# Performance work log

Hardware: AMD Instinct MI355X
Metric: run time of the kernel (lower is better)

Reference implementation:

```python
import jax, jax.numpy as jnp
import numpy as np

L = 64      # lattice side
H = 32      # hiddenSize
D = 2       # inputDim (spin states)
B = 1024    # batch of configurations
LOG_PROB_FACTOR = 0.5


def setup_inputs() -> dict:
    key = jax.random.key(0)
    ks = jax.random.split(key, 6)
    s = 0.3  # uniform init half-width (mimics variance_scaling uniform)
    return {
        "x": jax.random.randint(ks[0], (B, L, L), 0, D, dtype=jnp.int32),
        "Win": jax.random.uniform(ks[1], (2 * D, H), minval=-s, maxval=s, dtype=jnp.float32),
        "WcH": jax.random.uniform(ks[2], (H, H), minval=-s, maxval=s, dtype=jnp.float32),
        "WcV": jax.random.uniform(ks[3], (H, H), minval=-s, maxval=s, dtype=jnp.float32),
        "bV": jnp.zeros((H,), dtype=jnp.float32),
        "Wout": jax.random.uniform(ks[4], (H, D), minval=-s, maxval=s, dtype=jnp.float32),
        "bout": (0.1 * jax.random.normal(ks[5], (D,))).astype(jnp.float32),
    }


def _rev(line, b, axis):
    # reverse_line: identity if direction b == 1 else flip along `axis`
    return jnp.where(b == 1, line, jnp.flip(line, axis=axis))


def reference(x, Win, WcH, WcV, bV, Wout, bout):
    Bn, Ln, _ = x.shape
    d = Wout.shape[1]
    h = WcH.shape[0]
    xoh = jax.nn.one_hot(x, d, dtype=Win.dtype)            # [B, L, L, d]
    direction = jnp.asarray(np.where(np.arange(Ln) % 2 == 0, 1, -1).astype(np.int32))

    def col_step(hcarry, cols):
        # hcarry: horizontal carry [B, h]; cols: (carryV [B,h], stateH [B,d], stateV [B,d])
        cV, sH, sV = cols
        newR = jnp.concatenate([sH, sV], axis=-1)          # [B, 2d]
        newC = jax.nn.elu(hcarry @ WcH + (cV @ WcV + bV) + newR @ Win)  # [B, h]
        out = newC @ Wout + bout                            # [B, d]
        return newC, (newC, jax.nn.log_softmax(out, axis=-1))

    def row_step(carry, inputs):
        carryV_grid, prevRow = carry                        # [B, L, h], [B, L, d]
        x_row, b = inputs                                   # [B, L, d], scalar direction
        cV_rev = _rev(carryV_grid, b, 1)
        x_rev = _rev(x_row, b, 1)
        prev_rev = _rev(prevRow, b, 1)
        # shifted previous-column state along scan direction
        stateH = jnp.concatenate(
            [jnp.zeros((Bn, 1, d), dtype=x_rev.dtype), x_rev], axis=1)[:, :-1]
        xs = (jnp.swapaxes(cV_rev, 0, 1),                   # [L, B, h]
              jnp.swapaxes(stateH, 0, 1),                   # [L, B, d]
              jnp.swapaxes(prev_rev, 0, 1))                 # [L, B, d]
        _, (carries, logsm) = jax.lax.scan(
            col_step, jnp.zeros((Bn, h), dtype=Win.dtype), xs)
        carries = jnp.swapaxes(carries, 0, 1)               # [B, L, h]
        logsm = jnp.swapaxes(logsm, 0, 1)                   # [B, L, d]
        logP = jnp.sum(_rev(logsm, b, 1) * x_row, axis=-1)  # [B, L]
        logP = jnp.nan_to_num(logP, nan=-35.0)
        return (_rev(carries, b, 1), x_row), logP

    init = (jnp.zeros((Bn, Ln, h), dtype=Win.dtype),
            jnp.zeros((Bn, Ln, d), dtype=Win.dtype))
    _, probs = jax.lax.scan(row_step, init, (jnp.moveaxis(xoh, 1, 0), direction))
    # probs: [L_rows, B, L_cols] -> per-sample log-prob
    return LOG_PROB_FACTOR * jnp.sum(probs, axis=(0, 2))   # [B]
```

## Files before the change

### kernel.cpp

```cpp
#include <hip/hip_runtime.h>
#include <cstdint>

namespace {

typedef _Float16 half_t;
typedef half_t half8  __attribute__((ext_vector_type(8)));
typedef __fp16 fp16x2 __attribute__((ext_vector_type(2)));
typedef float  f32x4  __attribute__((ext_vector_type(4)));

constexpr int LSIDE = 64;
constexpr int HID   = 32;
constexpr int NB    = 16;

__device__ __forceinline__ half8 as_h8(uint4 u) { return __builtin_bit_cast(half8, u); }
__device__ __forceinline__ uint4 as_u4(half8 h) { return __builtin_bit_cast(uint4, h); }
__device__ __forceinline__ unsigned pk2(float a, float b) {
    fp16x2 t = __builtin_amdgcn_cvt_pkrtz(a, b);
    return __builtin_bit_cast(unsigned, t);
}
__device__ __forceinline__ float elu1(float v) {
    float e = __expf(v) - 1.f;
    return v > 0.f ? v : e;
}
__device__ __forceinline__ half8 elupack(const f32x4& a1, const f32x4& a2) {
    uint4 nb;
    nb.x = pk2(elu1(a1[0]), elu1(a1[1]));
    nb.y = pk2(elu1(a1[2]), elu1(a1[3]));
    nb.z = pk2(elu1(a2[0]), elu1(a2[1]));
    nb.w = pk2(elu1(a2[2]), elu1(a2[3]));
    return as_h8(nb);
}

#define MFMA(a,b,c) __builtin_amdgcn_mfma_f32_16x16x32_f16((a),(b),(c),0,0,0)


__global__ __launch_bounds__(192) void rnn2d_pipe3(
    const int*   __restrict__ x,
    const float* __restrict__ Win,
    const float* __restrict__ WcH,
    const float* __restrict__ WcV,
    const float* __restrict__ bV,
    const float* __restrict__ Wout,
    const float* __restrict__ bout,
    float*       __restrict__ out)
{
    const int tid = threadIdx.x;
    const int wv  = tid >> 6;
    const int l   = tid & 63;
    const int r_  = l & 15, g_ = l >> 4, n = l & 15;
    const int bbase = blockIdx.x * NB;

    __shared__ uint4 cvs[64 * 64];
    __shared__ f32x4 ring1[4 * 8 * 64];
    __shared__ f32x4 ring2[4 * 8 * 64];
    __shared__ uint4 h7buf[8 * 64];

    for (int i = tid; i < 64 * 64; i += 192) cvs[i] = uint4{0u,0u,0u,0u};

    const int j1 = 8 * (r_ >> 2) + (r_ & 3), j2 = j1 + 4;
    half8 A1h, A2h, A1v, A2v, A3a, A3b, Awd;
#pragma unroll
    for (int e = 0; e < 8; ++e) {
        const int k = 8 * g_ + e;
        A1h[e] = (half_t)WcH[k * HID + j1];
        A2h[e] = (half_t)WcH[k * HID + j2];
        A1v[e] = (half_t)WcV[k * HID + j1];
        A2v[e] = (half_t)WcV[k * HID + j2];
        float a3a = 0.f, a3b = 0.f;
        if (k < 4)       { a3a = Win[k * HID + j1]; a3b = Win[k * HID + j2]; }
        else if (k == 4) { a3a = bV[j1];            a3b = bV[j2]; }
        A3a[e] = (half_t)a3a;
        A3b[e] = (half_t)a3b;
        Awd[e] = (half_t)((r_ == 0) ? (Wout[k * 2 + 1] - Wout[k * 2 + 0]) : 0.f);
    }
    const float db = bout[1] - bout[0];
    f32x4 dinit; dinit[0]=db; dinit[1]=db; dinit[2]=db; dinit[3]=db;
    f32x4 zc;    zc[0]=0.f;  zc[1]=0.f;  zc[2]=0.f;  zc[3]=0.f;
    const unsigned gm16 = (g_ == 0) ? 0x3C00u : 0u;

    const int* xw = x + (long)bbase * 4096;

    __syncthreads();

    unsigned long long rmc = 0ull, rm1 = 0ull;
    int xr[NB];
    float logp = 0.f;
    f32x4 Ua[4], Ub[4];
    half8 hc = as_h8(uint4{0u,0u,0u,0u});
    uint4 h7[8];
#pragma unroll
    for (int i = 0; i < 8; ++i) h7[i] = uint4{0u,0u,0u,0u};

    if (wv >= 1) {
#pragma unroll
        for (int nn = 0; nn < NB; ++nn) xr[nn] = xw[nn * 4096 + l];
        {
            unsigned long long rm = 0ull;
#pragma unroll
            for (int nn = 0; nn < NB; ++nn) {
                unsigned long long bal = __ballot(xr[nn] == 1);
                rm = (n == nn) ? bal : rm;
            }
            rmc = rm;
        }
#pragma unroll
        for (int nn = 0; nn < NB; ++nn) xr[nn] = xw[nn * 4096 + 64 + l];
    }

    if (wv == 1) {
#pragma unroll
        for (int i = 0; i < 8; ++i) {
            unsigned aP = 0u;
            if (i > 0) {
                unsigned bl = (unsigned)((rmc >> (i - 1)) & 1ull);
                aP = gm16 << (bl << 4);
            }
            uint4 b3u{aP, 0u, gm16, 0u};
            ring1[(0*8 + i)*64 + l] = MFMA(A3a, as_h8(b3u), zc);
            ring2[(0*8 + i)*64 + l] = MFMA(A3b, as_h8(b3u), zc);
        }
#pragma unroll
        for (int i = 0; i < 8; ++i) {
            const int c = 8 + i;
            unsigned bl = (unsigned)((rmc >> (c - 1)) & 1ull);
            unsigned aP = gm16 << (bl << 4);
            uint4 b3u{aP, 0u, gm16, 0u};
            ring1[(1*8 + i)*64 + l] = MFMA(A3a, as_h8(b3u), zc);
            ring2[(1*8 + i)*64 + l] = MFMA(A3b, as_h8(b3u), zc);
        }
    }
    __syncthreads();

    if (wv == 0) {
        Ua[0] = ring1[0*64+l]; Ub[0] = ring2[0*64+l];
        Ua[1] = ring1[1*64+l]; Ub[1] = ring2[1*64+l];
        Ua[2] = ring1[2*64+l]; Ub[2] = ring2[2*64+l];
    }

    int c0 = 0, dir0 = 1;

#define PF(i)  { const int pf_=(i)+3; const int cs_=(gph+(pf_>>3))&3; const int ci_=pf_&7; \
                 Ua[((i)+3)&3] = ring1[(cs_*8+ci_)*64+l];                                  \
                 Ub[((i)+3)&3] = ring2[(cs_*8+ci_)*64+l]; }

#define NORMAL(i) { PF(i)                                                                  \
      f32x4 a1 = MFMA(A1h, hc, Ua[(i)&3]); f32x4 a2 = MFMA(A2h, hc, Ub[(i)&3]);           \
      hc = elupack(a1, a2); cvs[c0*64+l] = as_u4(hc); c0 += dir0; }

#define NORM7(i) { PF(i)                                                                   \
      f32x4 a1 = MFMA(A1h, hc, Ua[(i)&3]); f32x4 a2 = MFMA(A2h, hc, Ub[(i)&3]);           \
      hc = elupack(a1, a2); { uint4 u_ = as_u4(hc); cvs[c0*64+l] = u_; h7[(i)] = u_;      \
      h7buf[(i)*64+l] = u_; } c0 += dir0; }

#define SPECIAL(i) { PF(i)                                                                 \
      f32x4 p1 = MFMA(A1v, as_h8(h7[7-(i)]), Ua[(i)&3]);                                   \
      f32x4 p2 = MFMA(A2v, as_h8(h7[7-(i)]), Ub[(i)&3]);                                   \
      f32x4 a1 = MFMA(A1h, hc, p1); f32x4 a2 = MFMA(A2h, hc, p2);                          \
      hc = elupack(a1, a2); cvs[c0*64+l] = as_u4(hc); c0 += dir0; }

    for (int gph = 0; gph < 512; ++gph) {
        if (wv == 0) {
            const int k = gph & 7, rr = gph >> 3;
            if (k == 0) {
                dir0 = (rr & 1) ? -1 : 1;
                c0   = (rr & 1) ? 63 : 0;
                hc   = as_h8(uint4{0u,0u,0u,0u});
                SPECIAL(0) SPECIAL(1) SPECIAL(2) SPECIAL(3)
                SPECIAL(4) SPECIAL(5) SPECIAL(6) SPECIAL(7)
            } else if (k < 7) {
                NORMAL(0) NORMAL(1) NORMAL(2) NORMAL(3)
                NORMAL(4) NORMAL(5) NORMAL(6) NORMAL(7)
            } else {
                NORM7(0) NORM7(1) NORM7(2) NORM7(3)
                NORM7(4) NORM7(5) NORM7(6) NORM7(7)
            }
        } else if (wv == 1) {
            const int t = gph + 2;
            if (t < 512) {
                const int rp = t >> 3, kp = t & 7;
                const int dirp = (rp & 1) ? -1 : 1;
                const int slot = t & 3;
                if (kp == 0) {
                    rm1 = rmc;
                    {
                        unsigned long long rm = 0ull;
#pragma unroll
                        for (int nn = 0; nn < NB; ++nn) {
                            unsigned long long bal = __ballot(xr[nn] == 1);
                            rm = (n == nn) ? bal : rm;
                        }
                        rmc = rm;
                    }
                    const int nr = (rp < 63) ? rp + 1 : 63;
#pragma unroll
                    for (int nn = 0; nn < NB; ++nn) xr[nn] = xw[nn * 4096 + nr * 64 + l];
#pragma unroll
                    for (int i = 0; i < 8; ++i) {
                        const int c = (rp & 1) ? 63 - i : i;
                        unsigned aP = 0u;
                        if (i > 0) {
                            unsigned bl = (unsigned)((rmc >> (c - dirp)) & 1ull);
                            aP = gm16 << (bl << 4);
                        }
                        unsigned bu = (unsigned)((rm1 >> c) & 1ull);
                        unsigned bP = gm16 << (bu << 4);
                        uint4 b3u{aP, bP, gm16, 0u};
                        ring1[(slot*8 + i)*64 + l] = MFMA(A3a, as_h8(b3u), zc);
                        ring2[(slot*8 + i)*64 + l] = MFMA(A3b, as_h8(b3u), zc);
                    }
                } else {
#pragma unroll
                    for (int i = 0; i < 8; ++i) {
                        const int sg = 8 * kp + i;
                        const int c = (rp & 1) ? 63 - sg : sg;
                        half8 cvh = as_h8(cvs[c*64 + l]);
                        unsigned bl = (unsigned)((rmc >> (c - dirp)) & 1ull);
                        unsigned aP = gm16 << (bl << 4);
                        unsigned bP = 0u;
                        if (rp >= 1) {
                            unsigned bu = (unsigned)((rm1 >> c) & 1ull);
                            bP = gm16 << (bu << 4);
                        }
                        uint4 b3u{aP, bP, gm16, 0u};
                        f32x4 q1 = MFMA(A3a, as_h8(b3u), zc);
                        f32x4 q2 = MFMA(A3b, as_h8(b3u), zc);
                        ring1[(slot*8 + i)*64 + l] = MFMA(A1v, cvh, q1);
                        ring2[(slot*8 + i)*64 + l] = MFMA(A2v, cvh, q2);
                    }
                }
            }
        } else {
            const int t = gph + 2;
            if (t < 512) {
                const int rp = t >> 3, kp = t & 7;
                if (kp == 0) {
                    rm1 = rmc;
                    {
                        unsigned long long rm = 0ull;
#pragma unroll
                        for (int nn = 0; nn < NB; ++nn) {
                            unsigned long long bal = __ballot(xr[nn] == 1);
                            rm = (n == nn) ? bal : rm;
                        }
                        rmc = rm;
                    }
                    const int nr = (rp < 63) ? rp + 1 : 63;
#pragma unroll
                    for (int nn = 0; nn < NB; ++nn) xr[nn] = xw[nn * 4096 + nr * 64 + l];
                } else if (rp >= 1) {
                    f32x4 odv[8];
#pragma unroll
                    for (int i = 0; i < 8; ++i) {
                        const int sg = 8 * kp + i;
                        const int c = (rp & 1) ? 63 - sg : sg;
                        odv[i] = MFMA(Awd, as_h8(cvs[c*64 + l]), dinit);
                    }
#pragma unroll
                    for (int i = 0; i < 8; ++i) {
                        const int sg = 8 * kp + i;
                        const int c = (rp & 1) ? 63 - sg : sg;
                        unsigned s32 = (unsigned)((rm1 >> c) & 1ull) << 31;
                        float du = __int_as_float(__float_as_int(odv[i][0]) ^ s32);
                        logp -= __logf(1.f + __expf(du));
                    }
                    if (kp == 2) {
                        f32x4 odt[8];
#pragma unroll
                        for (int i = 0; i < 8; ++i)
                            odt[i] = MFMA(Awd, as_h8(h7buf[i*64 + l]), dinit);
#pragma unroll
                        for (int i = 0; i < 8; ++i) {
                            const int c = ((rp - 1) & 1) ? 7 - i : 56 + i;
                            unsigned s32 = (unsigned)((rm1 >> c) & 1ull) << 31;
                            float du = __int_as_float(__float_as_int(odt[i][0]) ^ s32);
                            logp -= __logf(1.f + __expf(du));
                        }
                    }
                }
            }
        }
        __syncthreads();
    }

    if (wv == 2) {
#pragma unroll 8
        for (int c = 0; c < 64; ++c) {
            f32x4 od = MFMA(Awd, as_h8(cvs[c*64 + l]), dinit);
            unsigned s32 = (unsigned)((rmc >> c) & 1ull) << 31;
            float du = __int_as_float(__float_as_int(od[0]) ^ s32);
            logp -= __logf(1.f + __expf(du));
        }
        if (l < NB) out[bbase + n] = 0.5f * logp;
    }

#undef PF
#undef NORMAL
#undef NORM7
#undef SPECIAL
}

}

extern "C" void kernel_launch(void* const* d_in, const int* in_sizes, int n_in,
                              void* d_out, int out_size, void* d_ws, size_t ws_size,
                              hipStream_t stream) {
    (void)n_in; (void)out_size; (void)d_ws; (void)ws_size;
    const int*   x    = (const int*)  d_in[0];
    const float* Win  = (const float*)d_in[1];
    const float* WcH  = (const float*)d_in[2];
    const float* WcV  = (const float*)d_in[3];
    const float* bV   = (const float*)d_in[4];
    const float* Wout = (const float*)d_in[5];
    const float* bout = (const float*)d_in[6];
    float*       out  = (float*)d_out;

    const int B = in_sizes[0] / (LSIDE * LSIDE);
    rnn2d_pipe3<<<B / NB, 192, 0, stream>>>(x, Win, WcH, WcV, bV, Wout, bout, out);
}
```

Before: 789.7 us.

## Store ELU state shifted by one and fold log2e scaling into weights

The hidden state is stored as s = (elu(v)+1)/ln2-scaled form so that the activation becomes max(v,0)*ln2 + exp2(min(v,0)), computed with a raw exp2 instruction and no select or subtract. The +1 offset and the log2e factor are folded into the weights, the biases (row sums subtracted) and the output bias, and the zero initial carries become ones. The aim is a shorter serial dependency chain in the recurrent critical path. The cost is a more intricate reparameterisation with fp16 rounding of shifted values and scaled weights, plus extra setup reads of the weights. The prefill of the first ring slots now also includes a vertical-carry MFMA over the ones-initialised cvs buffer.

After: 744.8 us. -5.7%, faster.

```diff
diff --git a/kernel.cpp b/kernel.cpp
--- a/kernel.cpp
+++ b/kernel.cpp
@@ -11,6 +11,8 @@
 constexpr int LSIDE = 64;
 constexpr int HID   = 32;
 constexpr int NB    = 16;
+constexpr float LOG2E = 1.4426950408889634f;
+constexpr float LN2   = 0.6931471805599453f;
 
 __device__ __forceinline__ half8 as_h8(uint4 u) { return __builtin_bit_cast(half8, u); }
 __device__ __forceinline__ uint4 as_u4(half8 h) { return __builtin_bit_cast(uint4, h); }
@@ -18,23 +20,27 @@
     fp16x2 t = __builtin_amdgcn_cvt_pkrtz(a, b);
     return __builtin_bit_cast(unsigned, t);
 }
-__device__ __forceinline__ float elu1(float v) {
-    float e = __expf(v) - 1.f;
-    return v > 0.f ? v : e;
-}
-__device__ __forceinline__ half8 elupack(const f32x4& a1, const f32x4& a2) {
+
+__device__ __forceinline__ half8 elupack2(const f32x4& a1, const f32x4& a2) {
+    float m[8], w[8], e[8], s[8];
+#pragma unroll
+    for (int i = 0; i < 4; ++i) { m[i]   = fmaxf(a1[i], 0.f); w[i]   = fminf(a1[i], 0.f); }
+#pragma unroll
+    for (int i = 0; i < 4; ++i) { m[4+i] = fmaxf(a2[i], 0.f); w[4+i] = fminf(a2[i], 0.f); }
+#pragma unroll
+    for (int i = 0; i < 8; ++i) e[i] = __builtin_amdgcn_exp2f(w[i]);
+#pragma unroll
+    for (int i = 0; i < 8; ++i) s[i] = fmaf(m[i], LN2, e[i]);
     uint4 nb;
-    nb.x = pk2(elu1(a1[0]), elu1(a1[1]));
-    nb.y = pk2(elu1(a1[2]), elu1(a1[3]));
-    nb.z = pk2(elu1(a2[0]), elu1(a2[1]));
-    nb.w = pk2(elu1(a2[2]), elu1(a2[3]));
+    nb.x = pk2(s[0], s[1]); nb.y = pk2(s[2], s[3]);
+    nb.z = pk2(s[4], s[5]); nb.w = pk2(s[6], s[7]);
     return as_h8(nb);
 }
 
 #define MFMA(a,b,c) __builtin_amdgcn_mfma_f32_16x16x32_f16((a),(b),(c),0,0,0)
 
 
-__global__ __launch_bounds__(192) void rnn2d_pipe3(
+__global__ __launch_bounds__(192) void rnn2d_pipe4(
     const int*   __restrict__ x,
     const float* __restrict__ Win,
     const float* __restrict__ WcH,
@@ -55,25 +61,36 @@
     __shared__ f32x4 ring2[4 * 8 * 64];
     __shared__ uint4 h7buf[8 * 64];
 
-    for (int i = tid; i < 64 * 64; i += 192) cvs[i] = uint4{0u,0u,0u,0u};
+    const uint4 ONES4{0x3C003C00u, 0x3C003C00u, 0x3C003C00u, 0x3C003C00u};
+    for (int i = tid; i < 64 * 64; i += 192) cvs[i] = ONES4;
 
     const int j1 = 8 * (r_ >> 2) + (r_ & 3), j2 = j1 + 4;
+    float rsH1 = 0.f, rsH2 = 0.f, rsV1 = 0.f, rsV2 = 0.f;
+#pragma unroll
+    for (int k = 0; k < HID; ++k) {
+        rsH1 += WcH[k * HID + j1]; rsH2 += WcH[k * HID + j2];
+        rsV1 += WcV[k * HID + j1]; rsV2 += WcV[k * HID + j2];
+    }
     half8 A1h, A2h, A1v, A2v, A3a, A3b, Awd;
 #pragma unroll
     for (int e = 0; e < 8; ++e) {
         const int k = 8 * g_ + e;
-        A1h[e] = (half_t)WcH[k * HID + j1];
-        A2h[e] = (half_t)WcH[k * HID + j2];
-        A1v[e] = (half_t)WcV[k * HID + j1];
-        A2v[e] = (half_t)WcV[k * HID + j2];
+        A1h[e] = (half_t)(LOG2E * WcH[k * HID + j1]);
+        A2h[e] = (half_t)(LOG2E * WcH[k * HID + j2]);
+        A1v[e] = (half_t)(LOG2E * WcV[k * HID + j1]);
+        A2v[e] = (half_t)(LOG2E * WcV[k * HID + j2]);
         float a3a = 0.f, a3b = 0.f;
         if (k < 4)       { a3a = Win[k * HID + j1]; a3b = Win[k * HID + j2]; }
-        else if (k == 4) { a3a = bV[j1];            a3b = bV[j2]; }
-        A3a[e] = (half_t)a3a;
-        A3b[e] = (half_t)a3b;
+        else if (k == 4) { a3a = bV[j1] - rsH1 - rsV1;
+                           a3b = bV[j2] - rsH2 - rsV2; }
+        A3a[e] = (half_t)(LOG2E * a3a);
+        A3b[e] = (half_t)(LOG2E * a3b);
         Awd[e] = (half_t)((r_ == 0) ? (Wout[k * 2 + 1] - Wout[k * 2 + 0]) : 0.f);
     }
-    const float db = bout[1] - bout[0];
+    float sAwd = 0.f;
+#pragma unroll
+    for (int k = 0; k < HID; ++k) sAwd += Wout[k * 2 + 1] - Wout[k * 2 + 0];
+    const float db = bout[1] - bout[0] - sAwd;
     f32x4 dinit; dinit[0]=db; dinit[1]=db; dinit[2]=db; dinit[3]=db;
     f32x4 zc;    zc[0]=0.f;  zc[1]=0.f;  zc[2]=0.f;  zc[3]=0.f;
     const unsigned gm16 = (g_ == 0) ? 0x3C00u : 0u;
@@ -86,10 +103,10 @@
     int xr[NB];
     float logp = 0.f;
     f32x4 Ua[4], Ub[4];
-    half8 hc = as_h8(uint4{0u,0u,0u,0u});
+    half8 hc = as_h8(ONES4);
     uint4 h7[8];
 #pragma unroll
-    for (int i = 0; i < 8; ++i) h7[i] = uint4{0u,0u,0u,0u};
+    for (int i = 0; i < 8; ++i) h7[i] = ONES4;
 
     if (wv >= 1) {
 #pragma unroll
@@ -125,8 +142,11 @@
             unsigned bl = (unsigned)((rmc >> (c - 1)) & 1ull);
             unsigned aP = gm16 << (bl << 4);
             uint4 b3u{aP, 0u, gm16, 0u};
-            ring1[(1*8 + i)*64 + l] = MFMA(A3a, as_h8(b3u), zc);
-            ring2[(1*8 + i)*64 + l] = MFMA(A3b, as_h8(b3u), zc);
+            f32x4 q1 = MFMA(A3a, as_h8(b3u), zc);
+            f32x4 q2 = MFMA(A3b, as_h8(b3u), zc);
+            half8 cvh = as_h8(cvs[c*64 + l]);
+            ring1[(1*8 + i)*64 + l] = MFMA(A1v, cvh, q1);
+            ring2[(1*8 + i)*64 + l] = MFMA(A2v, cvh, q2);
         }
     }
     __syncthreads();
@@ -145,18 +165,18 @@
 
 #define NORMAL(i) { PF(i)                                                                  \
       f32x4 a1 = MFMA(A1h, hc, Ua[(i)&3]); f32x4 a2 = MFMA(A2h, hc, Ub[(i)&3]);           \
-      hc = elupack(a1, a2); cvs[c0*64+l] = as_u4(hc); c0 += dir0; }
+      hc = elupack2(a1, a2); cvs[c0*64+l] = as_u4(hc); c0 += dir0; }
 
 #define NORM7(i) { PF(i)                                                                   \
       f32x4 a1 = MFMA(A1h, hc, Ua[(i)&3]); f32x4 a2 = MFMA(A2h, hc, Ub[(i)&3]);           \
-      hc = elupack(a1, a2); { uint4 u_ = as_u4(hc); cvs[c0*64+l] = u_; h7[(i)] = u_;      \
+      hc = elupack2(a1, a2); { uint4 u_ = as_u4(hc); cvs[c0*64+l] = u_; h7[(i)] = u_;     \
       h7buf[(i)*64+l] = u_; } c0 += dir0; }
 
 #define SPECIAL(i) { PF(i)                                                                 \
       f32x4 p1 = MFMA(A1v, as_h8(h7[7-(i)]), Ua[(i)&3]);                                   \
       f32x4 p2 = MFMA(A2v, as_h8(h7[7-(i)]), Ub[(i)&3]);                                   \
       f32x4 a1 = MFMA(A1h, hc, p1); f32x4 a2 = MFMA(A2h, hc, p2);                          \
-      hc = elupack(a1, a2); cvs[c0*64+l] = as_u4(hc); c0 += dir0; }
+      hc = elupack2(a1, a2); cvs[c0*64+l] = as_u4(hc); c0 += dir0; }
 
     for (int gph = 0; gph < 512; ++gph) {
         if (wv == 0) {
@@ -164,7 +184,7 @@
             if (k == 0) {
                 dir0 = (rr & 1) ? -1 : 1;
                 c0   = (rr & 1) ? 63 : 0;
-                hc   = as_h8(uint4{0u,0u,0u,0u});
+                hc   = as_h8(ONES4);
                 SPECIAL(0) SPECIAL(1) SPECIAL(2) SPECIAL(3)
                 SPECIAL(4) SPECIAL(5) SPECIAL(6) SPECIAL(7)
             } else if (k < 7) {
@@ -315,5 +335,5 @@
     float*       out  = (float*)d_out;
 
     const int B = in_sizes[0] / (LSIDE * LSIDE);
-    rnn2d_pipe3<<<B / NB, 192, 0, stream>>>(x, Win, WcH, WcV, bV, Wout, bout, out);
-}
+    rnn2d_pipe4<<<B / NB, 192, 0, stream>>>(x, Win, WcH, WcV, bV, Wout, bout, out);
+}
```
